# Optimization experiments

Measured on AMD Instinct MI355X. Metric: run time of the kernel, lower is better.

Reference implementation:

```python
import jax, jax.numpy as jnp
import numpy as np

P = 5            # assets (fixed by 5x5 MLP)
K = 4            # stacked layers
LB, UB = 0.0, 0.5
RF = 1.03
B = 524288       # batch size
ALPHA, OMEGA, BETA, MU = 0.1, 0.05, 0.05, 0.01
MAX_REBAL_ITERS = 8  # water-filling clamp loop converges in a few iters for P=5


def setup_inputs() -> dict:
    key = jax.random.key(0)
    k1, k2, k3, k4 = jax.random.split(key, 4)
    x1 = jax.random.uniform(k1, (B,), dtype=jnp.float32)                 # wealth per sample
    x2 = jax.random.uniform(k2, (B, P, P), dtype=jnp.float32)            # prev covariance
    eps = jax.random.normal(k3, (K, B, P), dtype=jnp.float32)            # N(0,I) draw per layer
    W = jax.random.normal(k4, (K, 3, P, P), dtype=jnp.float32) * 0.5     # 3 bias-free Linear(5,5) per layer
    return {"x1": x1, "x2": x2, "eps": eps, "W": W}


def _rebalance(w):
    """Vectorized clamp/redistribute loop over the whole batch. w: (B,P)."""
    old = w
    new = jnp.clip(w, LB, UB)
    done = jnp.zeros(w.shape[0], dtype=bool)

    def body(carry, _):
        old, new, done = carry
        leftover = jnp.sum(old - new, axis=1, keepdims=True)            # (B,1)
        masked = jnp.where(new != UB, new, 0.0)                          # non-capped weights
        new2 = new + leftover * masked / jnp.sum(masked, axis=1, keepdims=True)
        cont = jnp.any(new2 > UB, axis=1)                                # (B,)
        new3 = jnp.where(cont[:, None], jnp.clip(new2, LB, UB), new2)
        # freeze rows that already converged
        old_n = jnp.where(done[:, None], old, new2)
        new_n = jnp.where(done[:, None], new, new3)
        return (old_n, new_n, done | ~cont), None

    (_, new, _), _ = jax.lax.scan(body, (old, new, done), None, length=MAX_REBAL_ITERS)
    return new


def reference(x1, x2, eps, W):
    # Replicates the original bug: every StackLayer consumes the ORIGINAL
    # (x1, x2); only the last layer's output is returned.
    for k in range(K):
        Ce = jnp.einsum('bij,bj->bi', x2, eps[k])                        # prev_cov @ eps, (B,P)
        curr_cov = OMEGA + ALPHA * x2 + BETA * (Ce ** 2)[:, None, :]     # (B,P,P), row-broadcast
        R = MU + Ce                                                      # (B,P)
        h = R
        for l in range(3):                                               # torch Linear: x @ W.T
            h = jnp.tanh(h @ W[k, l].T)
        wts = jax.nn.softmax(h, axis=1)
        wts = _rebalance(wts)
        wealth = jnp.sum(x1[:, None] * wts * (1.0 + R) * RF, axis=1)     # (B,)
    return wealth, curr_cov
```

## Files before the change

### kernel.cpp

```cpp
#include <hip/hip_runtime.h>
#include <cmath>

#define P 5
#define LBV 0.0f
#define UBV 0.5f
#define RFV 1.03f
#define ALPHA 0.1f
#define OMEGA 0.05f
#define BETA 0.05f
#define MU 0.01f
#define NTHR 256

#define AS1 __attribute__((address_space(1)))
#define AS3 __attribute__((address_space(3)))

__device__ __forceinline__ float fast_tanh(float x) {
    float ax = fabsf(x);
    float t  = __expf(-2.0f * ax);
    float r  = (1.0f - t) * __builtin_amdgcn_rcpf(1.0f + t);
    return copysignf(r, x);
}

__global__ __launch_bounds__(NTHR, 5) void portfolio_kernel(
    const float* __restrict__ x1,
    const float* __restrict__ x2,
    const float* __restrict__ eps,
    const float* __restrict__ W,
    float* __restrict__ out, int B)
{
    __shared__ alignas(16) float sX2[4 * 1600];
    __shared__ alignas(16) float sE[4 * 320];

    const int tid  = threadIdx.x;
    const int lane = tid & 63;
    const int wv   = tid >> 6;
    const int bw   = blockIdx.x * NTHR + wv * 64;

    float x1v = x1[bw + lane];

    const float* gx2  = x2 + (size_t)bw * (P * P);
    float*       ldsx = &sX2[wv * 1600];
    #pragma unroll
    for (int i = 0; i < 6; ++i)
        __builtin_amdgcn_global_load_lds((const AS1 void*)(gx2 + i * 256 + lane * 4),
                                         (AS3 void*)(ldsx + i * 256), 16, 0, 0);
    __builtin_amdgcn_global_load_lds((const AS1 void*)(gx2 + 1536 + lane),
                                     (AS3 void*)(ldsx + 1536), 4, 0, 0);

    const float* ge   = eps + (size_t)3 * B * P + (size_t)bw * P;
    float*       ldse = &sE[wv * 320];
    __builtin_amdgcn_global_load_lds((const AS1 void*)(ge + lane * 4),
                                     (AS3 void*)(ldse), 16, 0, 0);
    __builtin_amdgcn_global_load_lds((const AS1 void*)(ge + 256 + lane),
                                     (AS3 void*)(ldse + 256), 4, 0, 0);

    __builtin_amdgcn_sched_barrier(0);
    __builtin_amdgcn_s_waitcnt(0x0F70);
    __builtin_amdgcn_sched_barrier(0);

    float r2[P * P];
    #pragma unroll
    for (int i = 0; i < P * P; ++i) r2[i] = ldsx[lane * (P * P) + i];

    float e[P];
    #pragma unroll
    for (int j = 0; j < P; ++j) e[j] = ldse[lane * P + j];

    float Ce[P];
    #pragma unroll
    for (int i = 0; i < P; ++i) {
        float s = 0.0f;
        #pragma unroll
        for (int j = 0; j < P; ++j) s = fmaf(r2[i * P + j], e[j], s);
        Ce[i] = s;
    }

    float R[P], h[P];
    #pragma unroll
    for (int i = 0; i < P; ++i) { R[i] = MU + Ce[i]; h[i] = R[i]; }

    const float* Wl = W + 3 * 3 * P * P;
    #pragma unroll
    for (int l = 0; l < 3; ++l) {
        float hn[P];
        #pragma unroll
        for (int i = 0; i < P; ++i) {
            float s = 0.0f;
            #pragma unroll
            for (int j = 0; j < P; ++j) s = fmaf(h[j], Wl[l * P * P + i * P + j], s);
            hn[i] = fast_tanh(s);
        }
        #pragma unroll
        for (int i = 0; i < P; ++i) h[i] = hn[i];
    }

    float w[P], ssum = 0.0f;
    #pragma unroll
    for (int i = 0; i < P; ++i) { w[i] = __expf(h[i]); ssum += w[i]; }
    float rs = __builtin_amdgcn_rcpf(ssum);
    #pragma unroll
    for (int i = 0; i < P; ++i) w[i] *= rs;

    float oldv[P], nw[P];
    #pragma unroll
    for (int i = 0; i < P; ++i) {
        oldv[i] = w[i];
        nw[i]   = fminf(fmaxf(w[i], LBV), UBV);
    }
    #pragma unroll
    for (int it = 0; it < 8; ++it) {
        float leftover = 0.0f;
        #pragma unroll
        for (int i = 0; i < P; ++i) leftover += oldv[i] - nw[i];
        float mk[P], msum = 0.0f;
        #pragma unroll
        for (int i = 0; i < P; ++i) {
            mk[i] = (nw[i] != UBV) ? nw[i] : 0.0f;
            msum += mk[i];
        }
        float scale = leftover * __builtin_amdgcn_rcpf(msum);
        float n2[P];
        #pragma unroll
        for (int i = 0; i < P; ++i) n2[i] = fmaf(scale, mk[i], nw[i]);
        bool cont = false;
        #pragma unroll
        for (int i = 0; i < P; ++i) cont = cont || (n2[i] > UBV);
        #pragma unroll
        for (int i = 0; i < P; ++i) {
            oldv[i] = n2[i];
            nw[i]   = cont ? fminf(fmaxf(n2[i], LBV), UBV) : n2[i];
        }
        if (!cont) break;
    }

    float ws = 0.0f;
    #pragma unroll
    for (int i = 0; i < P; ++i) ws = fmaf(nw[i], 1.0f + R[i], ws);
    out[bw + lane] = x1v * ws * RFV;

    float ce2[P];
    #pragma unroll
    for (int j = 0; j < P; ++j) ce2[j] = Ce[j] * Ce[j];
    #pragma unroll
    for (int i = 0; i < P; ++i) {
        #pragma unroll
        for (int j = 0; j < P; ++j)
            ldsx[lane * (P * P) + i * P + j] =
                fmaf(BETA, ce2[j], fmaf(ALPHA, r2[i * P + j], OMEGA));
    }

    float* gout = out + B + (size_t)bw * (P * P);
    const float4* s4 = (const float4*)ldsx;
    float4* g4 = (float4*)gout;
    #pragma unroll
    for (int r = 0; r < 6; ++r)
        g4[r * 64 + lane] = s4[r * 64 + lane];
    gout[1536 + lane] = ldsx[1536 + lane];
}

extern "C" void kernel_launch(void* const* d_in, const int* in_sizes, int n_in,
                              void* d_out, int out_size, void* d_ws, size_t ws_size,
                              hipStream_t stream) {
    const float* x1  = (const float*)d_in[0];
    const float* x2  = (const float*)d_in[1];
    const float* eps = (const float*)d_in[2];
    const float* W   = (const float*)d_in[3];
    float* out = (float*)d_out;
    const int B = in_sizes[0];
    const int blocks = B / NTHR;
    portfolio_kernel<<<blocks, NTHR, 0, stream>>>(x1, x2, eps, W, out, B);
}
```

Measured before the change: 136.1 us.

## Process four chunks per wave with double-buffered async LDS prefetch

Each wave now loops over four 64-sample chunks. It issues global-to-LDS loads for the next chunk into a second buffer while computing the current one, and the grid shrinks by the same factor. The aim is to hide global load latency behind compute within each wave. In exchange, LDS per block roughly doubles, launch bounds allow fewer blocks per CU, and the grid has far fewer blocks, which reduces occupancy and total parallelism on a bandwidth-bound kernel.

```diff
diff --git a/kernel.cpp b/kernel.cpp
--- a/kernel.cpp
+++ b/kernel.cpp
@@ -10,6 +10,7 @@
 #define BETA 0.05f
 #define MU 0.01f
 #define NTHR 256
+#define CPW 4
 
 #define AS1 __attribute__((address_space(1)))
 #define AS3 __attribute__((address_space(3)))
@@ -21,141 +22,158 @@
     return copysignf(r, x);
 }
 
-__global__ __launch_bounds__(NTHR, 5) void portfolio_kernel(
+__global__ __launch_bounds__(NTHR, 2) void portfolio_kernel(
     const float* __restrict__ x1,
     const float* __restrict__ x2,
     const float* __restrict__ eps,
     const float* __restrict__ W,
     float* __restrict__ out, int B)
 {
-    __shared__ alignas(16) float sX2[4 * 1600];
-    __shared__ alignas(16) float sE[4 * 320];
+    __shared__ alignas(16) float sBuf[4][2][1920];
 
     const int tid  = threadIdx.x;
     const int lane = tid & 63;
     const int wv   = tid >> 6;
-    const int bw   = blockIdx.x * NTHR + wv * 64;
+    const int s0   = blockIdx.x * (4 * CPW * 64) + wv * (CPW * 64);
+    const float* epsl = eps + (size_t)3 * B * P;
 
-    float x1v = x1[bw + lane];
+    auto issue = [&](int c, int buf) -> float {
+        const int sc = s0 + c * 64;
+        float xv = x1[sc + lane];
+        const float* gx2 = x2 + (size_t)sc * (P * P);
+        float* ldsx = &sBuf[wv][buf][0];
+        #pragma unroll
+        for (int i = 0; i < 6; ++i)
+            __builtin_amdgcn_global_load_lds((const AS1 void*)(gx2 + i * 256 + lane * 4),
+                                             (AS3 void*)(ldsx + i * 256), 16, 0, 0);
+        __builtin_amdgcn_global_load_lds((const AS1 void*)(gx2 + 1536 + lane),
+                                         (AS3 void*)(ldsx + 1536), 4, 0, 0);
+        const float* ge = epsl + (size_t)sc * P;
+        float* ldse = &sBuf[wv][buf][1600];
+        __builtin_amdgcn_global_load_lds((const AS1 void*)(ge + lane * 4),
+                                         (AS3 void*)(ldse), 16, 0, 0);
+        __builtin_amdgcn_global_load_lds((const AS1 void*)(ge + 256 + lane),
+                                         (AS3 void*)(ldse + 256), 4, 0, 0);
+        return xv;
+    };
 
-    const float* gx2  = x2 + (size_t)bw * (P * P);
-    float*       ldsx = &sX2[wv * 1600];
+    float x1cur = issue(0, 0);
+    float x1nxt = 0.0f;
+
     #pragma unroll
-    for (int i = 0; i < 6; ++i)
-        __builtin_amdgcn_global_load_lds((const AS1 void*)(gx2 + i * 256 + lane * 4),
-                                         (AS3 void*)(ldsx + i * 256), 16, 0, 0);
-    __builtin_amdgcn_global_load_lds((const AS1 void*)(gx2 + 1536 + lane),
-                                     (AS3 void*)(ldsx + 1536), 4, 0, 0);
+    for (int c = 0; c < CPW; ++c) {
+        const int buf = c & 1;
+        if (c + 1 < CPW) x1nxt = issue(c + 1, (c + 1) & 1);
 
-    const float* ge   = eps + (size_t)3 * B * P + (size_t)bw * P;
-    float*       ldse = &sE[wv * 320];
-    __builtin_amdgcn_global_load_lds((const AS1 void*)(ge + lane * 4),
-                                     (AS3 void*)(ldse), 16, 0, 0);
-    __builtin_amdgcn_global_load_lds((const AS1 void*)(ge + 256 + lane),
-                                     (AS3 void*)(ldse + 256), 4, 0, 0);
+        __builtin_amdgcn_sched_barrier(0);
+        if (c + 1 < CPW) __builtin_amdgcn_s_waitcnt(0x0F7A);
+        else             __builtin_amdgcn_s_waitcnt(0x0F78);
+        __builtin_amdgcn_sched_barrier(0);
 
-    __builtin_amdgcn_sched_barrier(0);
-    __builtin_amdgcn_s_waitcnt(0x0F70);
-    __builtin_amdgcn_sched_barrier(0);
+        float* ldsx = &sBuf[wv][buf][0];
+        float* ldse = &sBuf[wv][buf][1600];
+        const int sc = s0 + c * 64;
 
-    float r2[P * P];
-    #pragma unroll
-    for (int i = 0; i < P * P; ++i) r2[i] = ldsx[lane * (P * P) + i];
+        float r2[P * P];
+        #pragma unroll
+        for (int i = 0; i < P * P; ++i) r2[i] = ldsx[lane * (P * P) + i];
+        float e[P];
+        #pragma unroll
+        for (int j = 0; j < P; ++j) e[j] = ldse[lane * P + j];
 
-    float e[P];
-    #pragma unroll
-    for (int j = 0; j < P; ++j) e[j] = ldse[lane * P + j];
-
-    float Ce[P];
-    #pragma unroll
-    for (int i = 0; i < P; ++i) {
-        float s = 0.0f;
-        #pragma unroll
-        for (int j = 0; j < P; ++j) s = fmaf(r2[i * P + j], e[j], s);
-        Ce[i] = s;
-    }
-
-    float R[P], h[P];
-    #pragma unroll
-    for (int i = 0; i < P; ++i) { R[i] = MU + Ce[i]; h[i] = R[i]; }
-
-    const float* Wl = W + 3 * 3 * P * P;
-    #pragma unroll
-    for (int l = 0; l < 3; ++l) {
-        float hn[P];
+        float Ce[P];
         #pragma unroll
         for (int i = 0; i < P; ++i) {
             float s = 0.0f;
             #pragma unroll
-            for (int j = 0; j < P; ++j) s = fmaf(h[j], Wl[l * P * P + i * P + j], s);
-            hn[i] = fast_tanh(s);
+            for (int j = 0; j < P; ++j) s = fmaf(r2[i * P + j], e[j], s);
+            Ce[i] = s;
+        }
+
+        float R[P], h[P];
+        #pragma unroll
+        for (int i = 0; i < P; ++i) { R[i] = MU + Ce[i]; h[i] = R[i]; }
+
+        const float* Wl = W + 3 * 3 * P * P;
+        #pragma unroll
+        for (int l = 0; l < 3; ++l) {
+            float hn[P];
+            #pragma unroll
+            for (int i = 0; i < P; ++i) {
+                float s = 0.0f;
+                #pragma unroll
+                for (int j = 0; j < P; ++j) s = fmaf(h[j], Wl[l * P * P + i * P + j], s);
+                hn[i] = fast_tanh(s);
+            }
+            #pragma unroll
+            for (int i = 0; i < P; ++i) h[i] = hn[i];
+        }
+
+        float w[P], ssum = 0.0f;
+        #pragma unroll
+        for (int i = 0; i < P; ++i) { w[i] = __expf(h[i]); ssum += w[i]; }
+        float rs = __builtin_amdgcn_rcpf(ssum);
+        #pragma unroll
+        for (int i = 0; i < P; ++i) w[i] *= rs;
+
+        float oldv[P], nw[P];
+        #pragma unroll
+        for (int i = 0; i < P; ++i) {
+            oldv[i] = w[i];
+            nw[i]   = fminf(fmaxf(w[i], LBV), UBV);
         }
         #pragma unroll
-        for (int i = 0; i < P; ++i) h[i] = hn[i];
-    }
+        for (int it = 0; it < 8; ++it) {
+            float leftover = 0.0f;
+            #pragma unroll
+            for (int i = 0; i < P; ++i) leftover += oldv[i] - nw[i];
+            float mk[P], msum = 0.0f;
+            #pragma unroll
+            for (int i = 0; i < P; ++i) {
+                mk[i] = (nw[i] != UBV) ? nw[i] : 0.0f;
+                msum += mk[i];
+            }
+            float scale = leftover * __builtin_amdgcn_rcpf(msum);
+            float n2[P];
+            #pragma unroll
+            for (int i = 0; i < P; ++i) n2[i] = fmaf(scale, mk[i], nw[i]);
+            bool cont = false;
+            #pragma unroll
+            for (int i = 0; i < P; ++i) cont = cont || (n2[i] > UBV);
+            #pragma unroll
+            for (int i = 0; i < P; ++i) {
+                oldv[i] = n2[i];
+                nw[i]   = cont ? fminf(fmaxf(n2[i], LBV), UBV) : n2[i];
+            }
+            if (!cont) break;
+        }
 
-    float w[P], ssum = 0.0f;
-    #pragma unroll
-    for (int i = 0; i < P; ++i) { w[i] = __expf(h[i]); ssum += w[i]; }
-    float rs = __builtin_amdgcn_rcpf(ssum);
-    #pragma unroll
-    for (int i = 0; i < P; ++i) w[i] *= rs;
+        float ws = 0.0f;
+        #pragma unroll
+        for (int i = 0; i < P; ++i) ws = fmaf(nw[i], 1.0f + R[i], ws);
+        out[sc + lane] = x1cur * ws * RFV;
 
-    float oldv[P], nw[P];
-    #pragma unroll
-    for (int i = 0; i < P; ++i) {
-        oldv[i] = w[i];
-        nw[i]   = fminf(fmaxf(w[i], LBV), UBV);
-    }
-    #pragma unroll
-    for (int it = 0; it < 8; ++it) {
-        float leftover = 0.0f;
+        float ce2[P];
         #pragma unroll
-        for (int i = 0; i < P; ++i) leftover += oldv[i] - nw[i];
-        float mk[P], msum = 0.0f;
+        for (int j = 0; j < P; ++j) ce2[j] = Ce[j] * Ce[j];
         #pragma unroll
         for (int i = 0; i < P; ++i) {
-            mk[i] = (nw[i] != UBV) ? nw[i] : 0.0f;
-            msum += mk[i];
+            #pragma unroll
+            for (int j = 0; j < P; ++j)
+                ldsx[lane * (P * P) + i * P + j] =
+                    fmaf(BETA, ce2[j], fmaf(ALPHA, r2[i * P + j], OMEGA));
         }
-        float scale = leftover * __builtin_amdgcn_rcpf(msum);
-        float n2[P];
+
+        float* gout = out + B + (size_t)sc * (P * P);
+        const float4* s4 = (const float4*)ldsx;
+        float4* g4 = (float4*)gout;
         #pragma unroll
-        for (int i = 0; i < P; ++i) n2[i] = fmaf(scale, mk[i], nw[i]);
-        bool cont = false;
-        #pragma unroll
-        for (int i = 0; i < P; ++i) cont = cont || (n2[i] > UBV);
-        #pragma unroll
-        for (int i = 0; i < P; ++i) {
-            oldv[i] = n2[i];
-            nw[i]   = cont ? fminf(fmaxf(n2[i], LBV), UBV) : n2[i];
-        }
-        if (!cont) break;
+        for (int r = 0; r < 6; ++r)
+            g4[r * 64 + lane] = s4[r * 64 + lane];
+        gout[1536 + lane] = ldsx[1536 + lane];
+
+        x1cur = x1nxt;
     }
-
-    float ws = 0.0f;
-    #pragma unroll
-    for (int i = 0; i < P; ++i) ws = fmaf(nw[i], 1.0f + R[i], ws);
-    out[bw + lane] = x1v * ws * RFV;
-
-    float ce2[P];
-    #pragma unroll
-    for (int j = 0; j < P; ++j) ce2[j] = Ce[j] * Ce[j];
-    #pragma unroll
-    for (int i = 0; i < P; ++i) {
-        #pragma unroll
-        for (int j = 0; j < P; ++j)
-            ldsx[lane * (P * P) + i * P + j] =
-                fmaf(BETA, ce2[j], fmaf(ALPHA, r2[i * P + j], OMEGA));
-    }
-
-    float* gout = out + B + (size_t)bw * (P * P);
-    const float4* s4 = (const float4*)ldsx;
-    float4* g4 = (float4*)gout;
-    #pragma unroll
-    for (int r = 0; r < 6; ++r)
-        g4[r * 64 + lane] = s4[r * 64 + lane];
-    gout[1536 + lane] = ldsx[1536 + lane];
 }
 
 extern "C" void kernel_launch(void* const* d_in, const int* in_sizes, int n_in,
@@ -167,6 +185,6 @@
     const float* W   = (const float*)d_in[3];
     float* out = (float*)d_out;
     const int B = in_sizes[0];
-    const int blocks = B / NTHR;
+    const int blocks = B / (4 * CPW * 64);
     portfolio_kernel<<<blocks, NTHR, 0, stream>>>(x1, x2, eps, W, out, B);
 }
```

Result: no change. 136.3 us (+0.1%).
